# Kernel tuning notes

Hardware: AMD Instinct MI355X
Metric: run time of the kernel (lower is better)

## Reference

```python
import jax, jax.numpy as jnp
import numpy as np
from jax import lax

NUM_HEADS = 8
NUM_LAYERS = 3


def _conv3d(x, w, b):
    # x: [B,C,D,H,W], w: [O,I,3,3,3] (torch Conv3d layout), padding=1, stride=1
    y = lax.conv_general_dilated(x, w, window_strides=(1, 1, 1),
                                 padding=[(1, 1)] * 3,
                                 dimension_numbers=('NCDHW', 'OIDHW', 'NCDHW'))
    return y + b[None, :, None, None, None]


def _attn(x, wq, bq, wk, bk, wv, bv, gamma):
    # Faithful translation of MultiHeadAttentionModule.forward
    B, C, D, H, W = x.shape
    N = D * H * W
    hd = C // NUM_HEADS
    scale = jnp.asarray(hd ** 0.5, x.dtype)
    xf = x.reshape(B, C, N).transpose(0, 2, 1)  # [B,N,C]

    def proj(wm, bm):
        # torch Linear: y = x @ W.T + b ; split C -> (heads, head_dim)
        return (xf @ wm.T + bm).reshape(B, N, NUM_HEADS, hd).transpose(0, 2, 1, 3)

    q = proj(wq, bq)  # [B,h,N,d]
    k = proj(wk, bk)
    v = proj(wv, bv)
    energy = jnp.einsum('bhnd,bhmd->bhnm', q, k) / scale  # [B,h,N,N]
    attn = jax.nn.softmax(energy, axis=-1)
    o = jnp.einsum('bhnm,bhmd->bhnd', attn, v)  # [B,h,N,d]
    # permute(0,1,3,2).view(in_shape): channel order is (head, head_dim)
    o = o.transpose(0, 1, 3, 2).reshape(B, C, D, H, W)
    return gamma * o + x


def setup_inputs() -> dict:
    key = jax.random.key(0)
    ks = jax.random.split(key, 16)
    B, Cin, D, H, W = 1, 64, 16, 16, 16
    Co = 128
    L = NUM_LAYERS
    s = 0.02
    return {
        'x': jax.random.normal(ks[0], (B, Cin, D, H, W), jnp.float32),
        'lateral_w': jax.random.normal(ks[1], (Co, Cin, 3, 3, 3), jnp.float32) * s,
        'lateral_b': jax.random.normal(ks[2], (Co,), jnp.float32) * s,
        'pos': jax.random.normal(ks[3], (1, Co, D, H, W), jnp.float32) * s,
        'qw': jax.random.normal(ks[4], (L, Co, Co), jnp.float32) * s,
        'qb': jax.random.normal(ks[5], (L, Co), jnp.float32) * s,
        'kw': jax.random.normal(ks[6], (L, Co, Co), jnp.float32) * s,
        'kb': jax.random.normal(ks[7], (L, Co), jnp.float32) * s,
        'vw': jax.random.normal(ks[8], (L, Co, Co), jnp.float32) * s,
        'vb': jax.random.normal(ks[9], (L, Co), jnp.float32) * s,
        'gamma': jnp.full((L,), 0.5, jnp.float32),
        'out_w': jax.random.normal(ks[10], (Co, Co, 3, 3, 3), jnp.float32) * s,  # ConvTranspose3d weight [in,out,k,k,k]
        'out_b': jax.random.normal(ks[11], (Co,), jnp.float32) * s,
    }


def reference(x, lateral_w, lateral_b, pos, qw, qb, kw, kb, vw, vb, gamma, out_w, out_b):
    # t_dim == 1 branch of FPN3DWithMultiHeadAttention.forward
    lat = _conv3d(x, lateral_w, lateral_b) + pos
    for i in range(NUM_LAYERS):
        lat = _attn(lat, qw[i], qb[i], kw[i], kb[i], vw[i], vb[i], gamma[i])
    # ConvTranspose3d(k=3, stride=1, pad=1) == Conv3d with spatially flipped,
    # channel-transposed kernel and padding k-1-p = 1
    w_eq = jnp.flip(out_w, axis=(2, 3, 4)).transpose(1, 0, 2, 3, 4)
    return _conv3d(lat, w_eq, out_b)
```

## Files before the change

kernel.cpp:

```cpp
#include <hip/hip_runtime.h>
#include <hip/hip_bf16.h>

#define NVOX 4096
#define CDIM 128

typedef __attribute__((ext_vector_type(8)))  short bf16x8;
typedef __attribute__((ext_vector_type(4)))  float f32x4;
typedef __attribute__((ext_vector_type(16))) float f32x16;

static __device__ __forceinline__ short f2bf(float f) {
    __hip_bfloat16 h = __float2bfloat16(f);
    union { __hip_bfloat16 h; short s; } u; u.h = h; return u.s;
}
static __device__ __forceinline__ float fexp2(float x) {
    return __builtin_amdgcn_exp2f(x);
}
__device__ __forceinline__ int permpos(int ci) {
    return (((ci >> 2) & 3) << 3) + (ci & 3) + ((ci & 16) >> 2) + ((ci >> 5) << 5);
}
__device__ __forceinline__ int invp(int p) {
    const int c = p >> 5, r = p & 31, g = (r >> 3) & 3, j = r & 7;
    return (c << 5) + (j < 4 ? (g << 2) + j : 16 + (g << 2) + (j - 4));
}
__device__ __forceinline__ int pos16(int d) {
    return (d & 3) | ((d & 4) << 1) | ((d & 8) >> 1);
}

__global__ __launch_bounds__(256) void pack_all(
    const float* __restrict__ x,  const float* __restrict__ lw,
    const float* __restrict__ qw, const float* __restrict__ kw, const float* __restrict__ vw,
    const float* __restrict__ ow,
    short* __restrict__ xp, short* __restrict__ wb1, short* __restrict__ wqkv, short* __restrict__ wb2,
    short* __restrict__ xp2)
{
    const int b = blockIdx.x;
    const int tid = threadIdx.x;
    if (b < 1458) {
        const int e = b * 256 + tid;
        if (e >= 5832 * 64) return;
        const int vp = e >> 6, p = e & 63;
        const int z = vp / 324, rem = vp - z * 324, y = rem / 18, xx = rem % 18;
        short val = 0;
        if (z >= 1 && z <= 16 && y >= 1 && y <= 16 && xx >= 1 && xx <= 16) {
            const int n = ((z - 1) * 16 + (y - 1)) * 16 + (xx - 1);
            val = f2bf(x[invp(p) * NVOX + n]);
        }
        xp[e] = val;
    } else if (b < 1458 + 864) {
        const int e = (b - 1458) * 256 + tid;
        if (e >= 27 * 128 * 64) return;
        const int t = e >> 13, co = (e >> 6) & 127, p = e & 63;
        wb1[e] = f2bf(lw[(co * 64 + invp(p)) * 27 + t]);
    } else if (b < 1458 + 864 + 576) {
        const int e = (b - 2322) * 256 + tid;
        if (e >= 3 * 3 * 128 * 128) return;
        const int l = e / 49152, r = e - l * 49152;
        const int m = r >> 14, co = (r >> 7) & 127, p = r & 127;
        const float* W = (m == 0 ? qw : m == 1 ? kw : vw) + l * 16384;
        wqkv[e] = f2bf(W[co * 128 + invp(p)]);
    } else if (b < 1458 + 864 + 576 + 1728) {
        const int e = (b - 2898) * 256 + tid;
        if (e >= 27 * 128 * 128) return;
        const int t = e >> 14, co = (e >> 7) & 127, p = e & 127;
        wb2[e] = f2bf(ow[(invp(p) * 128 + co) * 27 + (26 - t)]);
    } else {
        const int e = (b - 4626) * 256 + tid;
        if (e >= 5832 * 16) return;
        const int4 z4 = {0, 0, 0, 0};
        *reinterpret_cast<int4*>(xp2 + e * 8) = z4;
    }
}

__global__ __launch_bounds__(256) void conv1_mfma(
    const short* __restrict__ xp,
    const short* __restrict__ wb,
    const float* __restrict__ bias, const float* __restrict__ pos,
    float* __restrict__ lat, short* __restrict__ latbf)
{
    __shared__ short bl[324 * 72];
    const int tid = threadIdx.x;
    const int g = blockIdx.x;
    const int cot = g >> 6;
    const int vgrp = g & 63;
    const int r0 = vgrp * 4;
    const int z = r0 >> 4, y0 = r0 & 15;

    for (int i = tid; i < 2592; i += 256) {
        const int col = i >> 3, pc = i & 7;
        const int line = col / 18, xq = col - line * 18;
        const int dz = line / 6, yi = line - dz * 6;
        const int4 v = *reinterpret_cast<const int4*>(
            xp + (((z + dz) * 18 + (y0 + yi)) * 18 + xq) * 64 + pc * 8);
        const int slot = ((((pc >> 2) ^ col) & 1) << 5) + ((pc & 3) << 3);
        *reinterpret_cast<int4*>(&bl[col * 72 + slot]) = v;
    }
    __syncthreads();

    const int wid = tid >> 6, lane = tid & 63;
    const int lg = lane >> 4, lq = lane & 15;
    const int wc = wid >> 1, wv = wid & 1;
    const int co0 = cot * 32 + wc * 16;

    const short* pA = wb + (co0 + lq) * 64 + lg * 8;

    auto ldA = [&](int t, bf16x8* A) {
        const short* p = pA + t * 8192;
        #pragma unroll
        for (int c = 0; c < 2; ++c) A[c] = *reinterpret_cast<const bf16x8*>(p + c * 32);
    };

    f32x4 acc0 = {0.f,0.f,0.f,0.f}, acc1 = {0.f,0.f,0.f,0.f};

    auto comp = [&](int t, const bf16x8* A) {
        const int dz = t / 9, r9 = t - dz * 9, dy = r9 / 3, dx = r9 - dy * 3;
        #pragma unroll
        for (int ry = 0; ry < 2; ++ry) {
            const int col = (dz * 6 + wv * 2 + ry + dy) * 18 + dx + lq;
            const short* bp = &bl[col * 72 + (lg << 3)];
            #pragma unroll
            for (int c = 0; c < 2; ++c) {
                const bf16x8 b = *reinterpret_cast<const bf16x8*>(bp + (((c ^ col) & 1) << 5));
                if (ry == 0) acc0 = __builtin_amdgcn_mfma_f32_16x16x32_bf16(A[c], b, acc0, 0, 0, 0);
                else         acc1 = __builtin_amdgcn_mfma_f32_16x16x32_bf16(A[c], b, acc1, 0, 0, 0);
            }
        }
    };

    bf16x8 A0[2], A1[2];
    int t = 0;
    ldA(0, A0);
    while (true) {
        if (t + 1 < 27) ldA(t + 1, A1);
        comp(t, A0);
        if (++t >= 27) break;
        if (t + 1 < 27) ldA(t + 1, A0);
        comp(t, A1);
        if (++t >= 27) break;
    }

    #pragma unroll
    for (int ry = 0; ry < 2; ++ry) {
        const f32x4 a = ry ? acc1 : acc0;
        const int n = (r0 + wv * 2 + ry) * 16 + lq;
        short4 s4;
        #pragma unroll
        for (int i = 0; i < 4; ++i) {
            const int co = co0 + 4 * lg + i;
            const float v = a[i] + bias[co] + pos[co * NVOX + n];
            lat[co * NVOX + n] = v;
            ((short*)&s4)[i] = f2bf(v);
        }
        *reinterpret_cast<short4*>(latbf + n * 128 + permpos(co0 + 4 * lg)) = s4;
    }
}

__global__ __launch_bounds__(256) void proj_mfma(
    const short* __restrict__ latbf,
    const short* __restrict__ wl,
    const float* __restrict__ bq, const float* __restrict__ bk, const float* __restrict__ bv,
    short* __restrict__ qP, short* __restrict__ kP, short* __restrict__ vP)
{
    const int m = blockIdx.z;
    const int wid = threadIdx.x >> 6, lane = threadIdx.x & 63;
    const int lg = lane >> 4, lq = lane & 15;
    const int co0 = blockIdx.y * 16;
    const int row0 = (blockIdx.x * 4 + wid) * 2;

    const short* A = wl + m * 16384 + (co0 + lq) * 128 + lg * 8;
    bf16x8 Af[4];
    #pragma unroll
    for (int c = 0; c < 4; ++c) Af[c] = *reinterpret_cast<const bf16x8*>(A + c * 32);

    const short* Bp0 = latbf + (row0 * 16 + lq) * 128 + lg * 8;
    const short* Bp1 = Bp0 + 16 * 128;
    bf16x8 Bf0[4], Bf1[4];
    #pragma unroll
    for (int c = 0; c < 4; ++c) Bf0[c] = *reinterpret_cast<const bf16x8*>(Bp0 + c * 32);
    #pragma unroll
    for (int c = 0; c < 4; ++c) Bf1[c] = *reinterpret_cast<const bf16x8*>(Bp1 + c * 32);

    f32x4 a0a = {0.f,0.f,0.f,0.f}, a0b = a0a, a1a = a0a, a1b = a0a;
    a0a = __builtin_amdgcn_mfma_f32_16x16x32_bf16(Af[0], Bf0[0], a0a, 0, 0, 0);
    a1a = __builtin_amdgcn_mfma_f32_16x16x32_bf16(Af[0], Bf1[0], a1a, 0, 0, 0);
    a0b = __builtin_amdgcn_mfma_f32_16x16x32_bf16(Af[1], Bf0[1], a0b, 0, 0, 0);
    a1b = __builtin_amdgcn_mfma_f32_16x16x32_bf16(Af[1], Bf1[1], a1b, 0, 0, 0);
    a0a = __builtin_amdgcn_mfma_f32_16x16x32_bf16(Af[2], Bf0[2], a0a, 0, 0, 0);
    a1a = __builtin_amdgcn_mfma_f32_16x16x32_bf16(Af[2], Bf1[2], a1a, 0, 0, 0);
    a0b = __builtin_amdgcn_mfma_f32_16x16x32_bf16(Af[3], Bf0[3], a0b, 0, 0, 0);
    a1b = __builtin_amdgcn_mfma_f32_16x16x32_bf16(Af[3], Bf1[3], a1b, 0, 0, 0);

    const int h = blockIdx.y;
    #pragma unroll
    for (int rr = 0; rr < 2; ++rr) {
        const f32x4 acc = rr ? (a1a + a1b) : (a0a + a0b);
        const int row = row0 + rr;
        const int n = row * 16 + lq;
        if (m == 2) {
            const int col = row * 16 + pos16(lq);
            #pragma unroll
            for (int r = 0; r < 4; ++r) {
                const int d = lg * 4 + r;
                vP[(h * 17 + d) * NVOX + col] = f2bf(acc[r] + bv[co0 + d]);
            }
            if (lg == 0) vP[(h * 17 + 16) * NVOX + col] = (short)0x3F80;
        } else {
            const float* bias = (m == 0) ? bq : bk;
            const float S = (m == 0) ? 0.25f * 1.4426950408889634f : 1.f;
            const int pg = ((lg & 1) << 3) | ((lg & 2) << 1);
            short4 s4;
            #pragma unroll
            for (int r = 0; r < 4; ++r) {
                const int co = co0 + lg * 4 + r;
                ((short*)&s4)[r] = f2bf((acc[r] + bias[co]) * S);
            }
            short* dst = (m == 0) ? qP : kP;
            *reinterpret_cast<short4*>(dst + ((h << 12) + n) * 16 + pg) = s4;
        }
    }
}

__global__ __launch_bounds__(512) void attn_mfma(
    const short* __restrict__ qP, const short* __restrict__ kP, const short* __restrict__ vP,
    const float* __restrict__ latin, float* __restrict__ latout, short* __restrict__ outbf,
    const float* __restrict__ gamma, int layer, int last)
{
    __shared__ float smO[8][64][17];
    const int tid = threadIdx.x;
    const int wid = tid >> 6, lane = tid & 63;
    const int l5 = lane >> 5, lm = lane & 31;
    const int qg = wid >> 2, ksp = wid & 3;
    const int h = blockIdx.y;
    const int qbase = blockIdx.x * 128 + qg * 64;

    const bf16x8 qf0 = *reinterpret_cast<const bf16x8*>(
        qP + (((h << 12) + qbase + lm) << 4) + l5 * 8);
    const bf16x8 qf1 = *reinterpret_cast<const bf16x8*>(
        qP + (((h << 12) + qbase + 32 + lm) << 4) + l5 * 8);

    const short* kbase = kP + (((size_t)h) << 16);
    const int vrow = (lm & 16) ? 16 : lm;
    const short* vbase = vP + ((size_t)h * 17 + vrow) * NVOX + l5 * 8;

    f32x16 acc0 = {0.f,0.f,0.f,0.f,0.f,0.f,0.f,0.f,0.f,0.f,0.f,0.f,0.f,0.f,0.f,0.f};
    f32x16 acc1 = acc0;
    const f32x16 zero = acc0;

    bf16x8 kfA, v0A, v1A, kfB, v0B, v1B;
    auto LD = [&](int kc, bf16x8& kf, bf16x8& v0, bf16x8& v1) {
        kf = *reinterpret_cast<const bf16x8*>(kbase + ((kc + lm) << 4) + l5 * 8);
        v0 = *reinterpret_cast<const bf16x8*>(vbase + kc);
        v1 = *reinterpret_cast<const bf16x8*>(vbase + kc + 16);
    };
    auto COMP = [&](const bf16x8& kf, const bf16x8& v0, const bf16x8& v1) {
        const f32x16 S0 = __builtin_amdgcn_mfma_f32_32x32x16_bf16(kf, qf0, zero, 0, 0, 0);
        const f32x16 S1 = __builtin_amdgcn_mfma_f32_32x32x16_bf16(kf, qf1, zero, 0, 0, 0);
        short p0[16], p1[16];
        #pragma unroll
        for (int r = 0; r < 16; ++r) p0[r] = f2bf(fexp2(S0[r]));
        #pragma unroll
        for (int r = 0; r < 16; ++r) p1[r] = f2bf(fexp2(S1[r]));
        const bf16x8 pa00 = {p0[0],p0[1],p0[2],p0[3],p0[4],p0[5],p0[6],p0[7]};
        const bf16x8 pa01 = {p0[8],p0[9],p0[10],p0[11],p0[12],p0[13],p0[14],p0[15]};
        const bf16x8 pa10 = {p1[0],p1[1],p1[2],p1[3],p1[4],p1[5],p1[6],p1[7]};
        const bf16x8 pa11 = {p1[8],p1[9],p1[10],p1[11],p1[12],p1[13],p1[14],p1[15]};
        acc0 = __builtin_amdgcn_mfma_f32_32x32x16_bf16(pa00, v0, acc0, 0, 0, 0);
        acc0 = __builtin_amdgcn_mfma_f32_32x32x16_bf16(pa01, v1, acc0, 0, 0, 0);
        acc1 = __builtin_amdgcn_mfma_f32_32x32x16_bf16(pa10, v0, acc1, 0, 0, 0);
        acc1 = __builtin_amdgcn_mfma_f32_32x32x16_bf16(pa11, v1, acc1, 0, 0, 0);
    };

    int kc = ksp * 1024;
    int it = 0;
    LD(kc, kfA, v0A, v1A);
    while (true) {
        if (it + 1 < 32) LD(kc + 32, kfB, v0B, v1B);
        COMP(kfA, v0A, v1A);
        kc += 32;
        if (++it >= 32) break;
        if (it + 1 < 32) LD(kc + 32, kfA, v0A, v1A);
        COMP(kfB, v0B, v1B);
        kc += 32;
        if (++it >= 32) break;
    }

    if (lm <= 16) {
        #pragma unroll
        for (int r = 0; r < 16; ++r) {
            const int qrow = (r & 3) + 8 * (r >> 2) + 4 * l5;
            smO[wid][qrow][lm]      = acc0[r];
            smO[wid][32 + qrow][lm] = acc1[r];
        }
    }
    __syncthreads();

    const int q = tid >> 2;
    const int d0 = (tid & 3) * 4;
    const int g4 = (q >> 6) * 4, ql = q & 63;
    const float ls = smO[g4][ql][16] + smO[g4+1][ql][16] + smO[g4+2][ql][16] + smO[g4+3][ql][16];
    const float ginv = gamma[layer] / ls;
    const int n = blockIdx.x * 128 + q;
    short4 s4;
    #pragma unroll
    for (int dd = 0; dd < 4; ++dd) {
        const int d = d0 + dd;
        const float Ov = smO[g4][ql][d] + smO[g4+1][ql][d] + smO[g4+2][ql][d] + smO[g4+3][ql][d];
        const int c = (h << 4) + d;
        const float val = Ov * ginv + latin[c * NVOX + n];
        if (!last) latout[c * NVOX + n] = val;
        ((short*)&s4)[dd] = f2bf(val);
    }
    if (!last) {
        *reinterpret_cast<short4*>(outbf + n * 128 + permpos((h << 4) + d0)) = s4;
    } else {
        const int zq = n >> 8, yq = (n >> 4) & 15, xq = n & 15;
        const int vp = (zq + 1) * 324 + (yq + 1) * 18 + (xq + 1);
        *reinterpret_cast<short4*>(outbf + vp * 128 + permpos((h << 4) + d0)) = s4;
    }
}

__global__ __launch_bounds__(256) void conv2_mfma(
    const short* __restrict__ xp,
    const short* __restrict__ wb,
    const float* __restrict__ bias,
    float* __restrict__ out)
{
    __shared__ short bl[324 * 136];
    const int tid = threadIdx.x;
    const int g = blockIdx.x;
    const int cot = g >> 6;
    const int vgrp = g & 63;
    const int r0 = vgrp * 4;
    const int z = r0 >> 4, y0 = r0 & 15;

    for (int i = tid; i < 5184; i += 256) {
        const int col = i >> 4, pc = i & 15;
        const int line = col / 18, xq = col - line * 18;
        const int dz = line / 6, yi = line - dz * 6;
        const int4 v = *reinterpret_cast<const int4*>(
            xp + (((z + dz) * 18 + (y0 + yi)) * 18 + xq) * 128 + pc * 8);
        const int slot = ((((pc >> 2) ^ col) & 3) << 5) + ((pc & 3) << 3);
        *reinterpret_cast<int4*>(&bl[col * 136 + slot]) = v;
    }
    __syncthreads();

    const int wid = tid >> 6, lane = tid & 63;
    const int lg = lane >> 4, lq = lane & 15;
    const int wc = wid >> 1, wv = wid & 1;
    const int co0 = cot * 32 + wc * 16;

    const short* pA = wb + (co0 + lq) * 128 + lg * 8;

    auto ldA = [&](int t, bf16x8* A) {
        const short* p = pA + t * 16384;
        #pragma unroll
        for (int c = 0; c < 4; ++c) A[c] = *reinterpret_cast<const bf16x8*>(p + c * 32);
    };

    f32x4 acc0 = {0.f,0.f,0.f,0.f}, acc1 = {0.f,0.f,0.f,0.f};

    auto comp = [&](int t, const bf16x8* A) {
        const int dz = t / 9, r9 = t - dz * 9, dy = r9 / 3, dx = r9 - dy * 3;
        #pragma unroll
        for (int ry = 0; ry < 2; ++ry) {
            const int col = (dz * 6 + wv * 2 + ry + dy) * 18 + dx + lq;
            const short* bp = &bl[col * 136 + (lg << 3)];
            #pragma unroll
            for (int c = 0; c < 4; ++c) {
                const bf16x8 b = *reinterpret_cast<const bf16x8*>(bp + (((c ^ col) & 3) << 5));
                if (ry == 0) acc0 = __builtin_amdgcn_mfma_f32_16x16x32_bf16(A[c], b, acc0, 0, 0, 0);
                else         acc1 = __builtin_amdgcn_mfma_f32_16x16x32_bf16(A[c], b, acc1, 0, 0, 0);
            }
        }
    };

    bf16x8 A0[4], A1[4];
    int t = 0;
    ldA(0, A0);
    while (true) {
        if (t + 1 < 27) ldA(t + 1, A1);
        comp(t, A0);
        if (++t >= 27) break;
        if (t + 1 < 27) ldA(t + 1, A0);
        comp(t, A1);
        if (++t >= 27) break;
    }

    #pragma unroll
    for (int ry = 0; ry < 2; ++ry) {
        const f32x4 a = ry ? acc1 : acc0;
        const int n = (r0 + wv * 2 + ry) * 16 + lq;
        #pragma unroll
        for (int i = 0; i < 4; ++i) {
            const int co = co0 + 4 * lg + i;
            out[co * NVOX + n] = a[i] + bias[co];
        }
    }
}

extern "C" void kernel_launch(void* const* d_in, const int* in_sizes, int n_in,
                              void* d_out, int out_size, void* d_ws, size_t ws_size,
                              hipStream_t stream) {
    const float* x     = (const float*)d_in[0];
    const float* lw    = (const float*)d_in[1];
    const float* lb    = (const float*)d_in[2];
    const float* pos   = (const float*)d_in[3];
    const float* qw    = (const float*)d_in[4];
    const float* qb    = (const float*)d_in[5];
    const float* kw    = (const float*)d_in[6];
    const float* kb    = (const float*)d_in[7];
    const float* vw    = (const float*)d_in[8];
    const float* vb    = (const float*)d_in[9];
    const float* gamma = (const float*)d_in[10];
    const float* ow    = (const float*)d_in[11];
    const float* ob    = (const float*)d_in[12];

    float* latA  = (float*)d_ws;
    float* latB  = latA + 524288;
    short* latbf = (short*)(latB + 524288);
    short* qP    = latbf + 524288;
    short* kP    = qP + 524288;
    short* vP    = kP + 524288;
    short* xpad  = vP + 557056;
    short* xpad2 = xpad + 373248;
    short* wbf1  = xpad2 + 746496;
    short* wqkv  = wbf1 + 221184;
    short* wbf2  = wqkv + 442368;

    pack_all<<<4809, 256, 0, stream>>>(x, lw, qw, kw, vw, ow, xpad, wbf1, wqkv, wbf2, xpad2);

    conv1_mfma<<<256, 256, 0, stream>>>(xpad, wbf1, lb, pos, latA, latbf);

    float* cur = latA;
    float* nxt = latB;
    for (int i = 0; i < 3; ++i) {
        const int last = (i == 2);
        proj_mfma<<<dim3(32, 8, 3), 256, 0, stream>>>(
            latbf, wqkv + i * 49152, qb + i * 128, kb + i * 128, vb + i * 128, qP, kP, vP);
        attn_mfma<<<dim3(32, 8), 512, 0, stream>>>(
            qP, kP, vP, cur, nxt, last ? xpad2 : latbf, gamma, i, last);
        float* t = cur; cur = nxt; nxt = t;
    }

    conv2_mfma<<<256, 256, 0, stream>>>(xpad2, wbf2, ob, (float*)d_out);
}
```

Before: 126.8 us.

## Fuse all stages into one cooperative persistent kernel with grid syncs

Replaces the sequence of eight kernel launches (pack, conv1, three proj+attn pairs, conv2) with a single cooperative kernel of 256 blocks × 512 threads that separates stages with grid.sync(). The conv stages now split the 27 taps across two wave halves and reduce the partial sums through shared memory. The aim is to remove launch gaps and inter-kernel drain costs. In exchange, the pack and projection stages run on fewer threads using grid-stride loops, grid syncs add their own overhead, and the large shared-memory footprint plus launch bounds may limit occupancy.

```diff
diff --git a/kernel.cpp b/kernel.cpp
--- a/kernel.cpp
+++ b/kernel.cpp
@@ -1,5 +1,8 @@
 #include <hip/hip_runtime.h>
 #include <hip/hip_bf16.h>
+#include <hip/hip_cooperative_groups.h>
+
+namespace cg = cooperative_groups;
 
 #define NVOX 4096
 #define CDIM 128
@@ -26,18 +29,22 @@
     return (d & 3) | ((d & 4) << 1) | ((d & 8) >> 1);
 }
 
-__global__ __launch_bounds__(256) void pack_all(
-    const float* __restrict__ x,  const float* __restrict__ lw,
-    const float* __restrict__ qw, const float* __restrict__ kw, const float* __restrict__ vw,
-    const float* __restrict__ ow,
-    short* __restrict__ xp, short* __restrict__ wb1, short* __restrict__ wqkv, short* __restrict__ wb2,
-    short* __restrict__ xp2)
+__global__ __launch_bounds__(512, 2) void fused_all(
+    const float* x,  const float* lw, const float* lb, const float* pos,
+    const float* qw, const float* qb, const float* kw, const float* kb,
+    const float* vw, const float* vb, const float* gamma,
+    const float* ow, const float* ob,
+    float* out,
+    float* latA, float* latB, short* latbf, short* qP, short* kP, short* vP,
+    short* xpad, short* xpad2, short* wbf1, short* wqkv, short* wbf2)
 {
-    const int b = blockIdx.x;
+    cg::grid_group grid = cg::this_grid();
+    __shared__ __align__(16) char smem[104768];
     const int tid = threadIdx.x;
-    if (b < 1458) {
-        const int e = b * 256 + tid;
-        if (e >= 5832 * 64) return;
+    const int bid = blockIdx.x;
+    const int gtid = (bid << 9) + tid;
+
+    for (int e = gtid; e < 5832 * 64; e += 131072) {
         const int vp = e >> 6, p = e & 63;
         const int z = vp / 324, rem = vp - z * 324, y = rem / 18, xx = rem % 18;
         short val = 0;
@@ -45,354 +52,360 @@
             const int n = ((z - 1) * 16 + (y - 1)) * 16 + (xx - 1);
             val = f2bf(x[invp(p) * NVOX + n]);
         }
-        xp[e] = val;
-    } else if (b < 1458 + 864) {
-        const int e = (b - 1458) * 256 + tid;
-        if (e >= 27 * 128 * 64) return;
+        xpad[e] = val;
+    }
+    for (int e = gtid; e < 27 * 128 * 64; e += 131072) {
         const int t = e >> 13, co = (e >> 6) & 127, p = e & 63;
-        wb1[e] = f2bf(lw[(co * 64 + invp(p)) * 27 + t]);
-    } else if (b < 1458 + 864 + 576) {
-        const int e = (b - 2322) * 256 + tid;
-        if (e >= 3 * 3 * 128 * 128) return;
+        wbf1[e] = f2bf(lw[(co * 64 + invp(p)) * 27 + t]);
+    }
+    for (int e = gtid; e < 3 * 3 * 128 * 128; e += 131072) {
         const int l = e / 49152, r = e - l * 49152;
         const int m = r >> 14, co = (r >> 7) & 127, p = r & 127;
         const float* W = (m == 0 ? qw : m == 1 ? kw : vw) + l * 16384;
         wqkv[e] = f2bf(W[co * 128 + invp(p)]);
-    } else if (b < 1458 + 864 + 576 + 1728) {
-        const int e = (b - 2898) * 256 + tid;
-        if (e >= 27 * 128 * 128) return;
+    }
+    for (int e = gtid; e < 27 * 128 * 128; e += 131072) {
         const int t = e >> 14, co = (e >> 7) & 127, p = e & 127;
-        wb2[e] = f2bf(ow[(invp(p) * 128 + co) * 27 + (26 - t)]);
-    } else {
-        const int e = (b - 4626) * 256 + tid;
-        if (e >= 5832 * 16) return;
+        wbf2[e] = f2bf(ow[(invp(p) * 128 + co) * 27 + (26 - t)]);
+    }
+    for (int e = gtid; e < 5832 * 16; e += 131072) {
         const int4 z4 = {0, 0, 0, 0};
-        *reinterpret_cast<int4*>(xp2 + e * 8) = z4;
-    }
-}
-
-__global__ __launch_bounds__(256) void conv1_mfma(
-    const short* __restrict__ xp,
-    const short* __restrict__ wb,
-    const float* __restrict__ bias, const float* __restrict__ pos,
-    float* __restrict__ lat, short* __restrict__ latbf)
-{
-    __shared__ short bl[324 * 72];
-    const int tid = threadIdx.x;
-    const int g = blockIdx.x;
-    const int cot = g >> 6;
-    const int vgrp = g & 63;
-    const int r0 = vgrp * 4;
-    const int z = r0 >> 4, y0 = r0 & 15;
-
-    for (int i = tid; i < 2592; i += 256) {
-        const int col = i >> 3, pc = i & 7;
-        const int line = col / 18, xq = col - line * 18;
-        const int dz = line / 6, yi = line - dz * 6;
-        const int4 v = *reinterpret_cast<const int4*>(
-            xp + (((z + dz) * 18 + (y0 + yi)) * 18 + xq) * 64 + pc * 8);
-        const int slot = ((((pc >> 2) ^ col) & 1) << 5) + ((pc & 3) << 3);
-        *reinterpret_cast<int4*>(&bl[col * 72 + slot]) = v;
-    }
-    __syncthreads();
-
-    const int wid = tid >> 6, lane = tid & 63;
-    const int lg = lane >> 4, lq = lane & 15;
-    const int wc = wid >> 1, wv = wid & 1;
-    const int co0 = cot * 32 + wc * 16;
-
-    const short* pA = wb + (co0 + lq) * 64 + lg * 8;
-
-    auto ldA = [&](int t, bf16x8* A) {
-        const short* p = pA + t * 8192;
-        #pragma unroll
-        for (int c = 0; c < 2; ++c) A[c] = *reinterpret_cast<const bf16x8*>(p + c * 32);
-    };
-
-    f32x4 acc0 = {0.f,0.f,0.f,0.f}, acc1 = {0.f,0.f,0.f,0.f};
-
-    auto comp = [&](int t, const bf16x8* A) {
-        const int dz = t / 9, r9 = t - dz * 9, dy = r9 / 3, dx = r9 - dy * 3;
+        *reinterpret_cast<int4*>(xpad2 + e * 8) = z4;
+    }
+    grid.sync();
+
+    {
+        short* bl  = reinterpret_cast<short*>(smem);
+        float* smP = reinterpret_cast<float*>(smem + 46656);
+        const int cot = bid >> 6, vgrp = bid & 63;
+        const int r0v = vgrp * 4;
+        const int z = r0v >> 4, y0 = r0v & 15;
+
+        for (int i = tid; i < 2592; i += 512) {
+            const int col = i >> 3, pc = i & 7;
+            const int line = col / 18, xq = col - line * 18;
+            const int dz = line / 6, yi = line - dz * 6;
+            const int4 v = *reinterpret_cast<const int4*>(
+                xpad + (((z + dz) * 18 + (y0 + yi)) * 18 + xq) * 64 + pc * 8);
+            const int slot = ((((pc >> 2) ^ col) & 1) << 5) + ((pc & 3) << 3);
+            *reinterpret_cast<int4*>(&bl[col * 72 + slot]) = v;
+        }
+        __syncthreads();
+
+        const int wid = tid >> 6, lane = tid & 63;
+        const int lg = lane >> 4, lq = lane & 15;
+        const int sb = wid & 3, th = wid >> 2;
+        const int wc = sb >> 1, wv = sb & 1;
+        const int co0 = cot * 32 + wc * 16;
+        const short* pA = wbf1 + (co0 + lq) * 64 + lg * 8;
+
+        auto ldA = [&](int t, bf16x8* A) {
+            const short* p = pA + t * 8192;
+            A[0] = *reinterpret_cast<const bf16x8*>(p);
+            A[1] = *reinterpret_cast<const bf16x8*>(p + 32);
+        };
+        f32x4 acc0 = {0.f,0.f,0.f,0.f}, acc1 = {0.f,0.f,0.f,0.f};
+        auto comp = [&](int t, const bf16x8* A) {
+            const int dz = t / 9, r9 = t - dz * 9, dy = r9 / 3, dx = r9 - dy * 3;
+            #pragma unroll
+            for (int ry = 0; ry < 2; ++ry) {
+                const int col = (dz * 6 + wv * 2 + ry + dy) * 18 + dx + lq;
+                const short* bp = &bl[col * 72 + (lg << 3)];
+                #pragma unroll
+                for (int c = 0; c < 2; ++c) {
+                    const bf16x8 b = *reinterpret_cast<const bf16x8*>(bp + (((c ^ col) & 1) << 5));
+                    if (ry == 0) acc0 = __builtin_amdgcn_mfma_f32_16x16x32_bf16(A[c], b, acc0, 0, 0, 0);
+                    else         acc1 = __builtin_amdgcn_mfma_f32_16x16x32_bf16(A[c], b, acc1, 0, 0, 0);
+                }
+            }
+        };
+        const int t0 = th ? 14 : 0, t1 = th ? 27 : 14;
+        bf16x8 A0[2], A1[2];
+        int t = t0;
+        ldA(t, A0);
+        while (true) {
+            if (t + 1 < t1) ldA(t + 1, A1);
+            comp(t, A0);
+            if (++t >= t1) break;
+            if (t + 1 < t1) ldA(t + 1, A0);
+            comp(t, A1);
+            if (++t >= t1) break;
+        }
         #pragma unroll
         for (int ry = 0; ry < 2; ++ry) {
-            const int col = (dz * 6 + wv * 2 + ry + dy) * 18 + dx + lq;
-            const short* bp = &bl[col * 72 + (lg << 3)];
-            #pragma unroll
-            for (int c = 0; c < 2; ++c) {
-                const bf16x8 b = *reinterpret_cast<const bf16x8*>(bp + (((c ^ col) & 1) << 5));
-                if (ry == 0) acc0 = __builtin_amdgcn_mfma_f32_16x16x32_bf16(A[c], b, acc0, 0, 0, 0);
-                else         acc1 = __builtin_amdgcn_mfma_f32_16x16x32_bf16(A[c], b, acc1, 0, 0, 0);
-            }
-        }
-    };
-
-    bf16x8 A0[2], A1[2];
-    int t = 0;
-    ldA(0, A0);
-    while (true) {
-        if (t + 1 < 27) ldA(t + 1, A1);
-        comp(t, A0);
-        if (++t >= 27) break;
-        if (t + 1 < 27) ldA(t + 1, A0);
-        comp(t, A1);
-        if (++t >= 27) break;
-    }
-
-    #pragma unroll
-    for (int ry = 0; ry < 2; ++ry) {
-        const f32x4 a = ry ? acc1 : acc0;
-        const int n = (r0 + wv * 2 + ry) * 16 + lq;
+            const f32x4 a = ry ? acc1 : acc0;
+            const int v = (wv * 2 + ry) * 16 + lq;
+            #pragma unroll
+            for (int i2 = 0; i2 < 4; ++i2)
+                smP[(th * 32 + wc * 16 + 4 * lg + i2) * 65 + v] = a[i2];
+        }
+        __syncthreads();
+        const int v = tid >> 3, c0 = (tid & 7) * 4;
+        const int n = vgrp * 64 + v;
         short4 s4;
         #pragma unroll
-        for (int i = 0; i < 4; ++i) {
-            const int co = co0 + 4 * lg + i;
-            const float v = a[i] + bias[co] + pos[co * NVOX + n];
-            lat[co * NVOX + n] = v;
-            ((short*)&s4)[i] = f2bf(v);
-        }
-        *reinterpret_cast<short4*>(latbf + n * 128 + permpos(co0 + 4 * lg)) = s4;
-    }
-}
-
-__global__ __launch_bounds__(256) void proj_mfma(
-    const short* __restrict__ latbf,
-    const short* __restrict__ wl,
-    const float* __restrict__ bq, const float* __restrict__ bk, const float* __restrict__ bv,
-    short* __restrict__ qP, short* __restrict__ kP, short* __restrict__ vP)
-{
-    const int m = blockIdx.z;
-    const int wid = threadIdx.x >> 6, lane = threadIdx.x & 63;
-    const int lg = lane >> 4, lq = lane & 15;
-    const int co0 = blockIdx.y * 16;
-    const int row0 = (blockIdx.x * 4 + wid) * 2;
-
-    const short* A = wl + m * 16384 + (co0 + lq) * 128 + lg * 8;
-    bf16x8 Af[4];
-    #pragma unroll
-    for (int c = 0; c < 4; ++c) Af[c] = *reinterpret_cast<const bf16x8*>(A + c * 32);
-
-    const short* Bp0 = latbf + (row0 * 16 + lq) * 128 + lg * 8;
-    const short* Bp1 = Bp0 + 16 * 128;
-    bf16x8 Bf0[4], Bf1[4];
-    #pragma unroll
-    for (int c = 0; c < 4; ++c) Bf0[c] = *reinterpret_cast<const bf16x8*>(Bp0 + c * 32);
-    #pragma unroll
-    for (int c = 0; c < 4; ++c) Bf1[c] = *reinterpret_cast<const bf16x8*>(Bp1 + c * 32);
-
-    f32x4 a0a = {0.f,0.f,0.f,0.f}, a0b = a0a, a1a = a0a, a1b = a0a;
-    a0a = __builtin_amdgcn_mfma_f32_16x16x32_bf16(Af[0], Bf0[0], a0a, 0, 0, 0);
-    a1a = __builtin_amdgcn_mfma_f32_16x16x32_bf16(Af[0], Bf1[0], a1a, 0, 0, 0);
-    a0b = __builtin_amdgcn_mfma_f32_16x16x32_bf16(Af[1], Bf0[1], a0b, 0, 0, 0);
-    a1b = __builtin_amdgcn_mfma_f32_16x16x32_bf16(Af[1], Bf1[1], a1b, 0, 0, 0);
-    a0a = __builtin_amdgcn_mfma_f32_16x16x32_bf16(Af[2], Bf0[2], a0a, 0, 0, 0);
-    a1a = __builtin_amdgcn_mfma_f32_16x16x32_bf16(Af[2], Bf1[2], a1a, 0, 0, 0);
-    a0b = __builtin_amdgcn_mfma_f32_16x16x32_bf16(Af[3], Bf0[3], a0b, 0, 0, 0);
-    a1b = __builtin_amdgcn_mfma_f32_16x16x32_bf16(Af[3], Bf1[3], a1b, 0, 0, 0);
-
-    const int h = blockIdx.y;
-    #pragma unroll
-    for (int rr = 0; rr < 2; ++rr) {
-        const f32x4 acc = rr ? (a1a + a1b) : (a0a + a0b);
-        const int row = row0 + rr;
-        const int n = row * 16 + lq;
-        if (m == 2) {
-            const int col = row * 16 + pos16(lq);
-            #pragma unroll
-            for (int r = 0; r < 4; ++r) {
-                const int d = lg * 4 + r;
-                vP[(h * 17 + d) * NVOX + col] = f2bf(acc[r] + bv[co0 + d]);
-            }
-            if (lg == 0) vP[(h * 17 + 16) * NVOX + col] = (short)0x3F80;
-        } else {
-            const float* bias = (m == 0) ? bq : bk;
-            const float S = (m == 0) ? 0.25f * 1.4426950408889634f : 1.f;
-            const int pg = ((lg & 1) << 3) | ((lg & 2) << 1);
+        for (int i2 = 0; i2 < 4; ++i2) {
+            const int c = c0 + i2;
+            const int co = cot * 32 + c;
+            const float val = smP[c * 65 + v] + smP[(32 + c) * 65 + v] + lb[co] + pos[co * NVOX + n];
+            latA[co * NVOX + n] = val;
+            ((short*)&s4)[i2] = f2bf(val);
+        }
+        *reinterpret_cast<short4*>(latbf + n * 128 + permpos(cot * 32 + c0)) = s4;
+    }
+    grid.sync();
+
+    float* cur = latA;
+    float* nxt = latB;
+    for (int layer = 0; layer < 3; ++layer) {
+        {
+            const int wid = tid >> 6, lane = tid & 63;
+            const int lg = lane >> 4, lq = lane & 15;
+            const short* wl = wqkv + layer * 49152;
+            const float* bqL = qb + layer * 128;
+            const float* bkL = kb + layer * 128;
+            const float* bvL = vb + layer * 128;
+            for (int task = (bid << 3) + wid; task < 3072; task += 2048) {
+                const int m = task >> 10;
+                const int rem = task & 1023;
+                const int h = rem >> 7;
+                const int sub = rem & 127;
+                const int row0 = sub * 2;
+                const int co0 = h * 16;
+
+                const short* A = wl + m * 16384 + (co0 + lq) * 128 + lg * 8;
+                bf16x8 Af[4];
+                #pragma unroll
+                for (int c = 0; c < 4; ++c) Af[c] = *reinterpret_cast<const bf16x8*>(A + c * 32);
+
+                const short* Bp0 = latbf + (row0 * 16 + lq) * 128 + lg * 8;
+                const short* Bp1 = Bp0 + 16 * 128;
+                bf16x8 Bf0[4], Bf1[4];
+                #pragma unroll
+                for (int c = 0; c < 4; ++c) Bf0[c] = *reinterpret_cast<const bf16x8*>(Bp0 + c * 32);
+                #pragma unroll
+                for (int c = 0; c < 4; ++c) Bf1[c] = *reinterpret_cast<const bf16x8*>(Bp1 + c * 32);
+
+                f32x4 a0a = {0.f,0.f,0.f,0.f}, a0b = a0a, a1a = a0a, a1b = a0a;
+                a0a = __builtin_amdgcn_mfma_f32_16x16x32_bf16(Af[0], Bf0[0], a0a, 0, 0, 0);
+                a1a = __builtin_amdgcn_mfma_f32_16x16x32_bf16(Af[0], Bf1[0], a1a, 0, 0, 0);
+                a0b = __builtin_amdgcn_mfma_f32_16x16x32_bf16(Af[1], Bf0[1], a0b, 0, 0, 0);
+                a1b = __builtin_amdgcn_mfma_f32_16x16x32_bf16(Af[1], Bf1[1], a1b, 0, 0, 0);
+                a0a = __builtin_amdgcn_mfma_f32_16x16x32_bf16(Af[2], Bf0[2], a0a, 0, 0, 0);
+                a1a = __builtin_amdgcn_mfma_f32_16x16x32_bf16(Af[2], Bf1[2], a1a, 0, 0, 0);
+                a0b = __builtin_amdgcn_mfma_f32_16x16x32_bf16(Af[3], Bf0[3], a0b, 0, 0, 0);
+                a1b = __builtin_amdgcn_mfma_f32_16x16x32_bf16(Af[3], Bf1[3], a1b, 0, 0, 0);
+
+                #pragma unroll
+                for (int rr = 0; rr < 2; ++rr) {
+                    const f32x4 acc = rr ? (a1a + a1b) : (a0a + a0b);
+                    const int row = row0 + rr;
+                    const int n = row * 16 + lq;
+                    if (m == 2) {
+                        const int col = row * 16 + pos16(lq);
+                        #pragma unroll
+                        for (int r = 0; r < 4; ++r) {
+                            const int d = lg * 4 + r;
+                            vP[(h * 17 + d) * NVOX + col] = f2bf(acc[r] + bvL[co0 + d]);
+                        }
+                        if (lg == 0) vP[(h * 17 + 16) * NVOX + col] = (short)0x3F80;
+                    } else {
+                        const float* bias = (m == 0) ? bqL : bkL;
+                        const float S = (m == 0) ? 0.25f * 1.4426950408889634f : 1.f;
+                        const int pg = ((lg & 1) << 3) | ((lg & 2) << 1);
+                        short4 s4;
+                        #pragma unroll
+                        for (int r = 0; r < 4; ++r) {
+                            const int co = co0 + lg * 4 + r;
+                            ((short*)&s4)[r] = f2bf((acc[r] + bias[co]) * S);
+                        }
+                        short* dst = (m == 0) ? qP : kP;
+                        *reinterpret_cast<short4*>(dst + ((h << 12) + n) * 16 + pg) = s4;
+                    }
+                }
+            }
+        }
+        grid.sync();
+
+        {
+            float* smO = reinterpret_cast<float*>(smem);
+            const int wid = tid >> 6, lane = tid & 63;
+            const int l5 = lane >> 5, lm = lane & 31;
+            const int qg = wid >> 2, ksp = wid & 3;
+            const int h = bid >> 5;
+            const int qblk = bid & 31;
+            const int qbase = qblk * 128 + qg * 64;
+            const int last = (layer == 2);
+            short* outbf = last ? xpad2 : latbf;
+
+            const bf16x8 qf0 = *reinterpret_cast<const bf16x8*>(
+                qP + (((h << 12) + qbase + lm) << 4) + l5 * 8);
+            const bf16x8 qf1 = *reinterpret_cast<const bf16x8*>(
+                qP + (((h << 12) + qbase + 32 + lm) << 4) + l5 * 8);
+
+            const short* kbase = kP + (((size_t)h) << 16);
+            const int vrow = (lm & 16) ? 16 : lm;
+            const short* vbase = vP + ((size_t)h * 17 + vrow) * NVOX + l5 * 8;
+
+            f32x16 acc0 = {0.f,0.f,0.f,0.f,0.f,0.f,0.f,0.f,0.f,0.f,0.f,0.f,0.f,0.f,0.f,0.f};
+            f32x16 acc1 = acc0;
+            const f32x16 zero = acc0;
+
+            bf16x8 kfA, v0A, v1A, kfB, v0B, v1B;
+            auto LD = [&](int kc, bf16x8& kf, bf16x8& v0, bf16x8& v1) {
+                kf = *reinterpret_cast<const bf16x8*>(kbase + ((kc + lm) << 4) + l5 * 8);
+                v0 = *reinterpret_cast<const bf16x8*>(vbase + kc);
+                v1 = *reinterpret_cast<const bf16x8*>(vbase + kc + 16);
+            };
+            auto COMP = [&](const bf16x8& kf, const bf16x8& v0, const bf16x8& v1) {
+                const f32x16 S0 = __builtin_amdgcn_mfma_f32_32x32x16_bf16(kf, qf0, zero, 0, 0, 0);
+                const f32x16 S1 = __builtin_amdgcn_mfma_f32_32x32x16_bf16(kf, qf1, zero, 0, 0, 0);
+                short p0[16], p1[16];
+                #pragma unroll
+                for (int r = 0; r < 16; ++r) p0[r] = f2bf(fexp2(S0[r]));
+                #pragma unroll
+                for (int r = 0; r < 16; ++r) p1[r] = f2bf(fexp2(S1[r]));
+                const bf16x8 pa00 = {p0[0],p0[1],p0[2],p0[3],p0[4],p0[5],p0[6],p0[7]};
+                const bf16x8 pa01 = {p0[8],p0[9],p0[10],p0[11],p0[12],p0[13],p0[14],p0[15]};
+                const bf16x8 pa10 = {p1[0],p1[1],p1[2],p1[3],p1[4],p1[5],p1[6],p1[7]};
+                const bf16x8 pa11 = {p1[8],p1[9],p1[10],p1[11],p1[12],p1[13],p1[14],p1[15]};
+                acc0 = __builtin_amdgcn_mfma_f32_32x32x16_bf16(pa00, v0, acc0, 0, 0, 0);
+                acc0 = __builtin_amdgcn_mfma_f32_32x32x16_bf16(pa01, v1, acc0, 0, 0, 0);
+                acc1 = __builtin_amdgcn_mfma_f32_32x32x16_bf16(pa10, v0, acc1, 0, 0, 0);
+                acc1 = __builtin_amdgcn_mfma_f32_32x32x16_bf16(pa11, v1, acc1, 0, 0, 0);
+            };
+
+            int kc = ksp * 1024;
+            int it = 0;
+            LD(kc, kfA, v0A, v1A);
+            while (true) {
+                if (it + 1 < 32) LD(kc + 32, kfB, v0B, v1B);
+                COMP(kfA, v0A, v1A);
+                kc += 32;
+                if (++it >= 32) break;
+                if (it + 1 < 32) LD(kc + 32, kfA, v0A, v1A);
+                COMP(kfB, v0B, v1B);
+                kc += 32;
+                if (++it >= 32) break;
+            }
+
+            if (lm <= 16) {
+                #pragma unroll
+                for (int r = 0; r < 16; ++r) {
+                    const int qrow = (r & 3) + 8 * (r >> 2) + 4 * l5;
+                    smO[(wid * 64 + qrow) * 17 + lm]      = acc0[r];
+                    smO[(wid * 64 + 32 + qrow) * 17 + lm] = acc1[r];
+                }
+            }
+            __syncthreads();
+
+            const int q = tid >> 2;
+            const int d0 = (tid & 3) * 4;
+            const int g4 = (q >> 6) * 4, ql = q & 63;
+            const float ls = smO[((g4    ) * 64 + ql) * 17 + 16]
+                           + smO[((g4 + 1) * 64 + ql) * 17 + 16]
+                           + smO[((g4 + 2) * 64 + ql) * 17 + 16]
+                           + smO[((g4 + 3) * 64 + ql) * 17 + 16];
+            const float ginv = gamma[layer] / ls;
+            const int n = qblk * 128 + q;
             short4 s4;
             #pragma unroll
-            for (int r = 0; r < 4; ++r) {
-                const int co = co0 + lg * 4 + r;
-                ((short*)&s4)[r] = f2bf((acc[r] + bias[co]) * S);
-            }
-            short* dst = (m == 0) ? qP : kP;
-            *reinterpret_cast<short4*>(dst + ((h << 12) + n) * 16 + pg) = s4;
-        }
-    }
-}
-
-__global__ __launch_bounds__(512) void attn_mfma(
-    const short* __restrict__ qP, const short* __restrict__ kP, const short* __restrict__ vP,
-    const float* __restrict__ latin, float* __restrict__ latout, short* __restrict__ outbf,
-    const float* __restrict__ gamma, int layer, int last)
-{
-    __shared__ float smO[8][64][17];
-    const int tid = threadIdx.x;
-    const int wid = tid >> 6, lane = tid & 63;
-    const int l5 = lane >> 5, lm = lane & 31;
-    const int qg = wid >> 2, ksp = wid & 3;
-    const int h = blockIdx.y;
-    const int qbase = blockIdx.x * 128 + qg * 64;
-
-    const bf16x8 qf0 = *reinterpret_cast<const bf16x8*>(
-        qP + (((h << 12) + qbase + lm) << 4) + l5 * 8);
-    const bf16x8 qf1 = *reinterpret_cast<const bf16x8*>(
-        qP + (((h << 12) + qbase + 32 + lm) << 4) + l5 * 8);
-
-    const short* kbase = kP + (((size_t)h) << 16);
-    const int vrow = (lm & 16) ? 16 : lm;
-    const short* vbase = vP + ((size_t)h * 17 + vrow) * NVOX + l5 * 8;
-
-    f32x16 acc0 = {0.f,0.f,0.f,0.f,0.f,0.f,0.f,0.f,0.f,0.f,0.f,0.f,0.f,0.f,0.f,0.f};
-    f32x16 acc1 = acc0;
-    const f32x16 zero = acc0;
-
-    bf16x8 kfA, v0A, v1A, kfB, v0B, v1B;
-    auto LD = [&](int kc, bf16x8& kf, bf16x8& v0, bf16x8& v1) {
-        kf = *reinterpret_cast<const bf16x8*>(kbase + ((kc + lm) << 4) + l5 * 8);
-        v0 = *reinterpret_cast<const bf16x8*>(vbase + kc);
-        v1 = *reinterpret_cast<const bf16x8*>(vbase + kc + 16);
-    };
-    auto COMP = [&](const bf16x8& kf, const bf16x8& v0, const bf16x8& v1) {
-        const f32x16 S0 = __builtin_amdgcn_mfma_f32_32x32x16_bf16(kf, qf0, zero, 0, 0, 0);
-        const f32x16 S1 = __builtin_amdgcn_mfma_f32_32x32x16_bf16(kf, qf1, zero, 0, 0, 0);
-        short p0[16], p1[16];
-        #pragma unroll
-        for (int r = 0; r < 16; ++r) p0[r] = f2bf(fexp2(S0[r]));
-        #pragma unroll
-        for (int r = 0; r < 16; ++r) p1[r] = f2bf(fexp2(S1[r]));
-        const bf16x8 pa00 = {p0[0],p0[1],p0[2],p0[3],p0[4],p0[5],p0[6],p0[7]};
-        const bf16x8 pa01 = {p0[8],p0[9],p0[10],p0[11],p0[12],p0[13],p0[14],p0[15]};
-        const bf16x8 pa10 = {p1[0],p1[1],p1[2],p1[3],p1[4],p1[5],p1[6],p1[7]};
-        const bf16x8 pa11 = {p1[8],p1[9],p1[10],p1[11],p1[12],p1[13],p1[14],p1[15]};
-        acc0 = __builtin_amdgcn_mfma_f32_32x32x16_bf16(pa00, v0, acc0, 0, 0, 0);
-        acc0 = __builtin_amdgcn_mfma_f32_32x32x16_bf16(pa01, v1, acc0, 0, 0, 0);
-        acc1 = __builtin_amdgcn_mfma_f32_32x32x16_bf16(pa10, v0, acc1, 0, 0, 0);
-        acc1 = __builtin_amdgcn_mfma_f32_32x32x16_bf16(pa11, v1, acc1, 0, 0, 0);
-    };
-
-    int kc = ksp * 1024;
-    int it = 0;
-    LD(kc, kfA, v0A, v1A);
-    while (true) {
-        if (it + 1 < 32) LD(kc + 32, kfB, v0B, v1B);
-        COMP(kfA, v0A, v1A);
-        kc += 32;
-        if (++it >= 32) break;
-        if (it + 1 < 32) LD(kc + 32, kfA, v0A, v1A);
-        COMP(kfB, v0B, v1B);
-        kc += 32;
-        if (++it >= 32) break;
-    }
-
-    if (lm <= 16) {
-        #pragma unroll
-        for (int r = 0; r < 16; ++r) {
-            const int qrow = (r & 3) + 8 * (r >> 2) + 4 * l5;
-            smO[wid][qrow][lm]      = acc0[r];
-            smO[wid][32 + qrow][lm] = acc1[r];
-        }
-    }
-    __syncthreads();
-
-    const int q = tid >> 2;
-    const int d0 = (tid & 3) * 4;
-    const int g4 = (q >> 6) * 4, ql = q & 63;
-    const float ls = smO[g4][ql][16] + smO[g4+1][ql][16] + smO[g4+2][ql][16] + smO[g4+3][ql][16];
-    const float ginv = gamma[layer] / ls;
-    const int n = blockIdx.x * 128 + q;
-    short4 s4;
-    #pragma unroll
-    for (int dd = 0; dd < 4; ++dd) {
-        const int d = d0 + dd;
-        const float Ov = smO[g4][ql][d] + smO[g4+1][ql][d] + smO[g4+2][ql][d] + smO[g4+3][ql][d];
-        const int c = (h << 4) + d;
-        const float val = Ov * ginv + latin[c * NVOX + n];
-        if (!last) latout[c * NVOX + n] = val;
-        ((short*)&s4)[dd] = f2bf(val);
-    }
-    if (!last) {
-        *reinterpret_cast<short4*>(outbf + n * 128 + permpos((h << 4) + d0)) = s4;
-    } else {
-        const int zq = n >> 8, yq = (n >> 4) & 15, xq = n & 15;
-        const int vp = (zq + 1) * 324 + (yq + 1) * 18 + (xq + 1);
-        *reinterpret_cast<short4*>(outbf + vp * 128 + permpos((h << 4) + d0)) = s4;
-    }
-}
-
-__global__ __launch_bounds__(256) void conv2_mfma(
-    const short* __restrict__ xp,
-    const short* __restrict__ wb,
-    const float* __restrict__ bias,
-    float* __restrict__ out)
-{
-    __shared__ short bl[324 * 136];
-    const int tid = threadIdx.x;
-    const int g = blockIdx.x;
-    const int cot = g >> 6;
-    const int vgrp = g & 63;
-    const int r0 = vgrp * 4;
-    const int z = r0 >> 4, y0 = r0 & 15;
-
-    for (int i = tid; i < 5184; i += 256) {
-        const int col = i >> 4, pc = i & 15;
-        const int line = col / 18, xq = col - line * 18;
-        const int dz = line / 6, yi = line - dz * 6;
-        const int4 v = *reinterpret_cast<const int4*>(
-            xp + (((z + dz) * 18 + (y0 + yi)) * 18 + xq) * 128 + pc * 8);
-        const int slot = ((((pc >> 2) ^ col) & 3) << 5) + ((pc & 3) << 3);
-        *reinterpret_cast<int4*>(&bl[col * 136 + slot]) = v;
-    }
-    __syncthreads();
-
-    const int wid = tid >> 6, lane = tid & 63;
-    const int lg = lane >> 4, lq = lane & 15;
-    const int wc = wid >> 1, wv = wid & 1;
-    const int co0 = cot * 32 + wc * 16;
-
-    const short* pA = wb + (co0 + lq) * 128 + lg * 8;
-
-    auto ldA = [&](int t, bf16x8* A) {
-        const short* p = pA + t * 16384;
-        #pragma unroll
-        for (int c = 0; c < 4; ++c) A[c] = *reinterpret_cast<const bf16x8*>(p + c * 32);
-    };
-
-    f32x4 acc0 = {0.f,0.f,0.f,0.f}, acc1 = {0.f,0.f,0.f,0.f};
-
-    auto comp = [&](int t, const bf16x8* A) {
-        const int dz = t / 9, r9 = t - dz * 9, dy = r9 / 3, dx = r9 - dy * 3;
+            for (int dd = 0; dd < 4; ++dd) {
+                const int d = d0 + dd;
+                const float Ov = smO[((g4    ) * 64 + ql) * 17 + d]
+                               + smO[((g4 + 1) * 64 + ql) * 17 + d]
+                               + smO[((g4 + 2) * 64 + ql) * 17 + d]
+                               + smO[((g4 + 3) * 64 + ql) * 17 + d];
+                const int c = (h << 4) + d;
+                const float val = Ov * ginv + cur[c * NVOX + n];
+                if (!last) nxt[c * NVOX + n] = val;
+                ((short*)&s4)[dd] = f2bf(val);
+            }
+            if (!last) {
+                *reinterpret_cast<short4*>(outbf + n * 128 + permpos((h << 4) + d0)) = s4;
+            } else {
+                const int zq = n >> 8, yq = (n >> 4) & 15, xq = n & 15;
+                const int vp = (zq + 1) * 324 + (yq + 1) * 18 + (xq + 1);
+                *reinterpret_cast<short4*>(outbf + vp * 128 + permpos((h << 4) + d0)) = s4;
+            }
+        }
+        grid.sync();
+        float* t = cur; cur = nxt; nxt = t;
+    }
+
+    {
+        short* bl  = reinterpret_cast<short*>(smem);
+        float* smP = reinterpret_cast<float*>(smem + 88128);
+        const int cot = bid >> 6, vgrp = bid & 63;
+        const int r0v = vgrp * 4;
+        const int z = r0v >> 4, y0 = r0v & 15;
+
+        for (int i = tid; i < 5184; i += 512) {
+            const int col = i >> 4, pc = i & 15;
+            const int line = col / 18, xq = col - line * 18;
+            const int dz = line / 6, yi = line - dz * 6;
+            const int4 v = *reinterpret_cast<const int4*>(
+                xpad2 + (((z + dz) * 18 + (y0 + yi)) * 18 + xq) * 128 + pc * 8);
+            const int slot = ((((pc >> 2) ^ col) & 3) << 5) + ((pc & 3) << 3);
+            *reinterpret_cast<int4*>(&bl[col * 136 + slot]) = v;
+        }
+        __syncthreads();
+
+        const int wid = tid >> 6, lane = tid & 63;
+        const int lg = lane >> 4, lq = lane & 15;
+        const int sb = wid & 3, th = wid >> 2;
+        const int wc = sb >> 1, wv = sb & 1;
+        const int co0 = cot * 32 + wc * 16;
+        const short* pA = wbf2 + (co0 + lq) * 128 + lg * 8;
+
+        auto ldA = [&](int t, bf16x8* A) {
+            const short* p = pA + t * 16384;
+            #pragma unroll
+            for (int c = 0; c < 4; ++c) A[c] = *reinterpret_cast<const bf16x8*>(p + c * 32);
+        };
+        f32x4 acc0 = {0.f,0.f,0.f,0.f}, acc1 = {0.f,0.f,0.f,0.f};
+        auto comp = [&](int t, const bf16x8* A) {
+            const int dz = t / 9, r9 = t - dz * 9, dy = r9 / 3, dx = r9 - dy * 3;
+            #pragma unroll
+            for (int ry = 0; ry < 2; ++ry) {
+                const int col = (dz * 6 + wv * 2 + ry + dy) * 18 + dx + lq;
+                const short* bp = &bl[col * 136 + (lg << 3)];
+                #pragma unroll
+                for (int c = 0; c < 4; ++c) {
+                    const bf16x8 b = *reinterpret_cast<const bf16x8*>(bp + (((c ^ col) & 3) << 5));
+                    if (ry == 0) acc0 = __builtin_amdgcn_mfma_f32_16x16x32_bf16(A[c], b, acc0, 0, 0, 0);
+                    else         acc1 = __builtin_amdgcn_mfma_f32_16x16x32_bf16(A[c], b, acc1, 0, 0, 0);
+                }
+            }
+        };
+        const int t0 = th ? 14 : 0, t1 = th ? 27 : 14;
+        bf16x8 A0[4], A1[4];
+        int t = t0;
+        ldA(t, A0);
+        while (true) {
+            if (t + 1 < t1) ldA(t + 1, A1);
+            comp(t, A0);
+            if (++t >= t1) break;
+            if (t + 1 < t1) ldA(t + 1, A0);
+            comp(t, A1);
+            if (++t >= t1) break;
+        }
         #pragma unroll
         for (int ry = 0; ry < 2; ++ry) {
-            const int col = (dz * 6 + wv * 2 + ry + dy) * 18 + dx + lq;
-            const short* bp = &bl[col * 136 + (lg << 3)];
-            #pragma unroll
-            for (int c = 0; c < 4; ++c) {
-                const bf16x8 b = *reinterpret_cast<const bf16x8*>(bp + (((c ^ col) & 3) << 5));
-                if (ry == 0) acc0 = __builtin_amdgcn_mfma_f32_16x16x32_bf16(A[c], b, acc0, 0, 0, 0);
-                else         acc1 = __builtin_amdgcn_mfma_f32_16x16x32_bf16(A[c], b, acc1, 0, 0, 0);
-            }
-        }
-    };
-
-    bf16x8 A0[4], A1[4];
-    int t = 0;
-    ldA(0, A0);
-    while (true) {
-        if (t + 1 < 27) ldA(t + 1, A1);
-        comp(t, A0);
-        if (++t >= 27) break;
-        if (t + 1 < 27) ldA(t + 1, A0);
-        comp(t, A1);
-        if (++t >= 27) break;
-    }
-
-    #pragma unroll
-    for (int ry = 0; ry < 2; ++ry) {
-        const f32x4 a = ry ? acc1 : acc0;
-        const int n = (r0 + wv * 2 + ry) * 16 + lq;
+            const f32x4 a = ry ? acc1 : acc0;
+            const int v = (wv * 2 + ry) * 16 + lq;
+            #pragma unroll
+            for (int i2 = 0; i2 < 4; ++i2)
+                smP[(th * 32 + wc * 16 + 4 * lg + i2) * 65 + v] = a[i2];
+        }
+        __syncthreads();
+        const int v = tid >> 3, c0 = (tid & 7) * 4;
+        const int n = vgrp * 64 + v;
         #pragma unroll
-        for (int i = 0; i < 4; ++i) {
-            const int co = co0 + 4 * lg + i;
-            out[co * NVOX + n] = a[i] + bias[co];
+        for (int i2 = 0; i2 < 4; ++i2) {
+            const int c = c0 + i2;
+            const int co = cot * 32 + c;
+            out[co * NVOX + n] = smP[c * 65 + v] + smP[(32 + c) * 65 + v] + ob[co];
         }
     }
 }
@@ -413,6 +426,7 @@
     const float* gamma = (const float*)d_in[10];
     const float* ow    = (const float*)d_in[11];
     const float* ob    = (const float*)d_in[12];
+    float* outp        = (float*)d_out;
 
     float* latA  = (float*)d_ws;
     float* latB  = latA + 524288;
@@ -426,20 +440,14 @@
     short* wqkv  = wbf1 + 221184;
     short* wbf2  = wqkv + 442368;
 
-    pack_all<<<4809, 256, 0, stream>>>(x, lw, qw, kw, vw, ow, xpad, wbf1, wqkv, wbf2, xpad2);
-
-    conv1_mfma<<<256, 256, 0, stream>>>(xpad, wbf1, lb, pos, latA, latbf);
-
-    float* cur = latA;
-    float* nxt = latB;
-    for (int i = 0; i < 3; ++i) {
-        const int last = (i == 2);
-        proj_mfma<<<dim3(32, 8, 3), 256, 0, stream>>>(
-            latbf, wqkv + i * 49152, qb + i * 128, kb + i * 128, vb + i * 128, qP, kP, vP);
-        attn_mfma<<<dim3(32, 8), 512, 0, stream>>>(
-            qP, kP, vP, cur, nxt, last ? xpad2 : latbf, gamma, i, last);
-        float* t = cur; cur = nxt; nxt = t;
-    }
-
-    conv2_mfma<<<256, 256, 0, stream>>>(xpad2, wbf2, ob, (float*)d_out);
-}
+    void* args[] = {
+        (void*)&x, (void*)&lw, (void*)&lb, (void*)&pos,
+        (void*)&qw, (void*)&qb, (void*)&kw, (void*)&kb,
+        (void*)&vw, (void*)&vb, (void*)&gamma,
+        (void*)&ow, (void*)&ob, (void*)&outp,
+        (void*)&latA, (void*)&latB, (void*)&latbf, (void*)&qP, (void*)&kP, (void*)&vP,
+        (void*)&xpad, (void*)&xpad2, (void*)&wbf1, (void*)&wqkv, (void*)&wbf2
+    };
+    hipLaunchCooperativeKernel((const void*)fused_all, dim3(256), dim3(512),
+                               args, 0u, stream);
+}
```

Result: slower. 383.7 us (+202.6%).
